# Optimization experiments

Measured on AMD Instinct MI355X. Metric: run time of the kernel, lower is better.

The kernel has to match this reference:

```python
import jax, jax.numpy as jnp
import numpy as np

ALPHA = 0.1
BETA = 0.25


def setup_inputs() -> dict:
    key = jax.random.key(0)
    k1, k2 = jax.random.split(key)
    B, C, D = 65536, 4096, 128
    x = jax.random.normal(k1, (B, D), dtype=jnp.float32)
    codes = jax.random.normal(k2, (1, C, D), dtype=jnp.float32)
    return {"x": x, "codes": codes}


def reference(x, codes):
    # x: [B, D], codes: [1, C, D]
    D = x.shape[1]
    c = codes[0]  # [C, D]
    d2 = (
        jnp.sum(x * x, axis=1, keepdims=True)
        + jnp.sum(c * c, axis=1)[None, :]
        - 2.0 * (x @ c.T)
    )  # [B, C]
    distances = jnp.sqrt(jnp.maximum(d2, 0.0)) / (D ** 0.5) / ALPHA
    indices = jnp.argmin(distances, axis=-1)  # [B]
    quantized = c[indices]  # [B, D] codebook gather
    loss_commit = jnp.mean(
        jnp.sum((x - jax.lax.stop_gradient(quantized)) ** 2, axis=-1)
    )
    loss_codebook = jnp.mean(
        jnp.sum((quantized - jax.lax.stop_gradient(x)) ** 2, axis=-1)
    )
    loss = loss_commit + BETA * loss_codebook
    return quantized, indices, loss
```

## Files before the change

kernel.cpp:

```cpp
#include <hip/hip_runtime.h>

constexpr int Bn = 65536;
constexpr int Cn = 4096;
constexpr int Dn = 128;
constexpr float TAU = 0.055f;

typedef _Float16 v8h __attribute__((ext_vector_type(8)));
typedef float v16f __attribute__((ext_vector_type(16)));

#define MFMA16(a, b, c) __builtin_amdgcn_mfma_f32_32x32x16_f16((a), (b), (c), 0, 0, 0)

__global__ void pack_codes_kernel(const float* __restrict__ codes,
                                  float* __restrict__ cnorm,
                                  _Float16* __restrict__ pack,
                                  float* __restrict__ codesT,
                                  int* __restrict__ flagcount) {
  int tid = blockIdx.x * 256 + threadIdx.x;
  if (tid == 0) *flagcount = 0;
  int f = tid >> 6;
  int l = tid & 63;
  int ct = f / 9, s = f % 9;
  int code = (ct << 5) + (l & 31);
  if (s < 8) {
    int kb = (s << 4) + ((l >> 5) << 3);
    const float* p = codes + (size_t)code * Dn + kb;
    float4 a = ((const float4*)p)[0];
    float4 b = ((const float4*)p)[1];
    float v[8] = {a.x, a.y, a.z, a.w, b.x, b.y, b.z, b.w};
#pragma unroll
    for (int j = 0; j < 8; ++j)
      codesT[(size_t)(kb + j) * Cn + code] = v[j];
    v8h hi;
#pragma unroll
    for (int j = 0; j < 8; ++j) {
      float sv = -2.f * v[j];
      hi[j] = (_Float16)sv;
    }
    *(v8h*)(pack + (size_t)ct * 4608 + s * 512 + l * 8) = hi;
  } else {
    v8h a = {0, 0, 0, 0, 0, 0, 0, 0};
    if (l < 32) {
      const float4* p = (const float4*)(codes + (size_t)code * Dn);
      double sd = 0.0;
#pragma unroll
      for (int i = 0; i < Dn / 4; ++i) {
        float4 v = p[i];
        sd += (double)v.x * v.x + (double)v.y * v.y + (double)v.z * v.z +
              (double)v.w * v.w;
      }
      float cn = (float)sd;
      cnorm[code] = cn;
      float c5 = cn + 512.f;
      _Float16 h1 = (_Float16)c5;
      float r1 = c5 - (float)h1;
      _Float16 h2 = (_Float16)r1;
      float r2 = r1 - (float)h2;
      _Float16 h3 = (_Float16)r2;
      a[0] = h1;
      a[1] = h2;
      a[2] = h3;
    }
    *(v8h*)(pack + (size_t)ct * 4608 + 8 * 512 + l * 8) = a;
  }
}

__launch_bounds__(256, 4)
__global__ void argmin_mfma_kernel(const float* __restrict__ x,
                                   const _Float16* __restrict__ pack,
                                   float* __restrict__ pm1,
                                   float* __restrict__ pm2,
                                   float* __restrict__ pidx) {
  __shared__ __align__(16) _Float16 packLDS[4][4608];

  const int t = threadIdx.x;
  const int w = t >> 6;
  const int l = t & 63;
  const int h = blockIdx.x & 3;
  const int row0 = (blockIdx.x >> 2) * 256;

  v8h xh[2][8];
#pragma unroll
  for (int tt = 0; tt < 2; ++tt) {
#pragma unroll
    for (int ks = 0; ks < 8; ++ks) {
      int xrow = row0 + w * 64 + tt * 32 + (l & 31);
      int kb = ks * 16 + (l >> 5) * 8;
      const float* xp = x + (size_t)xrow * Dn + kb;
      float4 a = ((const float4*)xp)[0];
      float4 b = ((const float4*)xp)[1];
      float v[8] = {a.x, a.y, a.z, a.w, b.x, b.y, b.z, b.w};
      v8h hh;
#pragma unroll
      for (int j = 0; j < 8; ++j) hh[j] = (_Float16)v[j];
      xh[tt][ks] = hh;
    }
  }

  v8h bones;
#pragma unroll
  for (int j = 0; j < 8; ++j)
    bones[j] = (l < 32 && j < 3) ? (_Float16)1.0f : (_Float16)0.0f;

  v16f zacc;
#pragma unroll
  for (int i = 0; i < 16; ++i) zacc[i] = 0.f;

  const char* packbase = (const char*)pack + (size_t)(h * 32) * 9216;
  auto stage = [&](int pt, int bank) {
    const char* src = packbase + (size_t)pt * 18432 + l * 16;
    char* dstb = (char*)&packLDS[bank * 2][0];
    for (int i = w; i < 18; i += 4) {
      __builtin_amdgcn_global_load_lds(
          (const __attribute__((address_space(1))) unsigned*)(src + i * 1024),
          (__attribute__((address_space(3))) unsigned*)(dstb + i * 1024), 16,
          0, 0);
    }
  };

  stage(0, 0);
  __syncthreads();

  unsigned umin1[2] = {0xFFFFFFFFu, 0xFFFFFFFFu};
  unsigned umin2[2] = {0xFFFFFFFFu, 0xFFFFFFFFu};
  int idx[2] = {0, 0};

  auto update = [&](const v16f& a, int tt, int codebase) {
    unsigned b[16];
#pragma unroll
    for (int r = 0; r < 16; ++r)
      b[r] = (__float_as_uint(a[r]) & 0xFFFFFFF0u) | (unsigned)r;
    unsigned m1 = 0xFFFFFFFFu, m2 = 0xFFFFFFFFu;
#pragma unroll
    for (int i = 0; i < 8; ++i) {
      unsigned lo = min(b[2 * i], b[2 * i + 1]);
      unsigned hi = max(b[2 * i], b[2 * i + 1]);
      unsigned mx = max(m1, lo);
      m1 = min(m1, lo);
      m2 = min(min(m2, hi), mx);
    }
    unsigned r1 = m1 & 15u;
    int tidx = codebase + (int)(8 * (r1 >> 2) + (r1 & 3));
    bool lt = m1 < umin1[tt];
    umin2[tt] = lt ? min(umin1[tt], m2) : min(umin2[tt], m1);
    idx[tt] = lt ? tidx : idx[tt];
    umin1[tt] = lt ? m1 : umin1[tt];
  };

  for (int it = 0; it < 16; ++it) {
    const int bank = it & 1;
    if (it + 1 < 16) stage(it + 1, bank ^ 1);

#pragma unroll
    for (int j = 0; j < 2; ++j) {
      const _Float16* base = &packLDS[bank * 2 + j][l * 8];
      v8h a_cn = *(const v8h*)(base + 8 * 512);
      v16f ini = MFMA16(a_cn, bones, zacc);
      v8h a_h0 = *(const v8h*)(base + 0 * 512);
      v16f acc0 = MFMA16(a_h0, xh[0][0], ini);
      v16f acc1 = MFMA16(a_h0, xh[1][0], ini);
#pragma unroll
      for (int s = 1; s < 8; ++s) {
        v8h a_h = *(const v8h*)(base + s * 512);
        acc0 = MFMA16(a_h, xh[0][s], acc0);
        acc1 = MFMA16(a_h, xh[1][s], acc1);
      }
      const int codebase = h * 1024 + (2 * it + j) * 32 + 4 * (l >> 5);
      update(acc0, 0, codebase);
      update(acc1, 1, codebase);
    }
    __syncthreads();
  }

#pragma unroll
  for (int tt = 0; tt < 2; ++tt) {
    unsigned o1 = (unsigned)__shfl_xor((int)umin1[tt], 32);
    unsigned o2 = (unsigned)__shfl_xor((int)umin2[tt], 32);
    int oi = __shfl_xor(idx[tt], 32);
    bool sw = (o1 < umin1[tt]) || (o1 == umin1[tt] && oi < idx[tt]);
    unsigned n1 = sw ? o1 : umin1[tt];
    int ni = sw ? oi : idx[tt];
    unsigned big = sw ? umin1[tt] : o1;
    unsigned n2 = min(min(umin2[tt], o2), big);
    if (l < 32) {
      int row = row0 + w * 64 + tt * 32 + l;
      pm1[h * Bn + row] = __uint_as_float(n1 & 0xFFFFFFF0u);
      pm2[h * Bn + row] = __uint_as_float(n2 & 0xFFFFFFF0u);
      pidx[h * Bn + row] = (float)ni;
    }
  }
}

__global__ void merge_kernel(const float* __restrict__ pm1,
                             const float* __restrict__ pm2,
                             const float* __restrict__ pidx,
                             float* __restrict__ idxf,
                             int* __restrict__ flaglist,
                             int* __restrict__ flagcount) {
  int r = blockIdx.x * 256 + threadIdx.x;
  float m1 = pm1[r];
  float mw2 = pm2[r];
  float mi = pidx[r];
  float m2 = 3.4e38f;
#pragma unroll
  for (int h = 1; h < 4; ++h) {
    float v1 = pm1[h * Bn + r];
    float v2 = pm2[h * Bn + r];
    float vi = pidx[h * Bn + r];
    bool win = v1 < m1;
    m2 = fminf(m2, win ? m1 : v1);
    mw2 = win ? v2 : mw2;
    mi = win ? vi : mi;
    m1 = win ? v1 : m1;
  }
  m2 = fminf(m2, mw2);
  idxf[r] = mi;
  if (m2 - m1 < TAU) {
    int p = atomicAdd(flagcount, 1);
    flaglist[p] = r;
  }
}

__global__ void rescore_part_kernel(const float* __restrict__ x,
                                    const float* __restrict__ codesT,
                                    const float* __restrict__ cnorm,
                                    const int* __restrict__ flaglist,
                                    const int* __restrict__ flagcount,
                                    float* __restrict__ prv,
                                    int* __restrict__ pri) {
  __shared__ __align__(16) float xrow[Dn];
  __shared__ float wv[4];
  __shared__ int wis[4];
  const int t = threadIdx.x;
  const int total = 4 * (*flagcount);

  for (int wi = blockIdx.x; wi < total; wi += gridDim.x) {
    const int j = wi >> 2;
    const int q = wi & 3;
    const int r = flaglist[j];
    __syncthreads();
    if (t < 32) ((float4*)xrow)[t] = ((const float4*)(x + (size_t)r * Dn))[t];
    __syncthreads();

    const int c0 = q * 1024 + 4 * t;
    const float* cp = codesT + c0;
    float4 s = {0.f, 0.f, 0.f, 0.f};
#pragma unroll 4
    for (int d = 0; d < Dn; ++d) {
      float xv = xrow[d];
      float4 cv = *(const float4*)(cp + (size_t)d * Cn);
      s.x = fmaf(cv.x, xv, s.x);
      s.y = fmaf(cv.y, xv, s.y);
      s.z = fmaf(cv.z, xv, s.z);
      s.w = fmaf(cv.w, xv, s.w);
    }
    float k0 = fmaf(-2.f, s.x, cnorm[c0]);
    float k1 = fmaf(-2.f, s.y, cnorm[c0 + 1]);
    float k2 = fmaf(-2.f, s.z, cnorm[c0 + 2]);
    float k3 = fmaf(-2.f, s.w, cnorm[c0 + 3]);
    float bv = k0;
    int bi = c0;
    if (k1 < bv) { bv = k1; bi = c0 + 1; }
    if (k2 < bv) { bv = k2; bi = c0 + 2; }
    if (k3 < bv) { bv = k3; bi = c0 + 3; }
#pragma unroll
    for (int off = 32; off > 0; off >>= 1) {
      float ov = __shfl_down(bv, off);
      int oi = __shfl_down(bi, off);
      if (ov < bv || (ov == bv && oi < bi)) { bv = ov; bi = oi; }
    }
    if ((t & 63) == 0) { wv[t >> 6] = bv; wis[t >> 6] = bi; }
    __syncthreads();
    if (t == 0) {
#pragma unroll
      for (int k = 1; k < 4; ++k) {
        if (wv[k] < bv || (wv[k] == bv && wis[k] < bi)) {
          bv = wv[k];
          bi = wis[k];
        }
      }
      prv[wi] = bv;
      pri[wi] = bi;
    }
  }
}

__global__ void rescore_final_kernel(const int* __restrict__ flaglist,
                                     const int* __restrict__ flagcount,
                                     const float* __restrict__ prv,
                                     const int* __restrict__ pri,
                                     float* __restrict__ idxf) {
  const int cnt = *flagcount;
  for (int j = blockIdx.x * blockDim.x + threadIdx.x; j < cnt;
       j += gridDim.x * blockDim.x) {
    float bv = prv[4 * j];
    int bi = pri[4 * j];
#pragma unroll
    for (int k = 1; k < 4; ++k) {
      float ov = prv[4 * j + k];
      int oi = pri[4 * j + k];
      if (ov < bv || (ov == bv && oi < bi)) { bv = ov; bi = oi; }
    }
    idxf[flaglist[j]] = (float)bi;
  }
}

__global__ void gather_loss_kernel(const float* __restrict__ x,
                                   const float* __restrict__ codes,
                                   const float* __restrict__ idxf,
                                   float* __restrict__ quant,
                                   float* __restrict__ partial) {
  __shared__ float part[8];
  const int t = threadIdx.x;
  const int wave = t >> 6;
  const int lane = t & 63;
  const int half = lane >> 5;
  const int l = lane & 31;
  const int base = blockIdx.x * 32;

  float s = 0.f;
#pragma unroll
  for (int pass = 0; pass < 4; ++pass) {
    int row = base + pass * 8 + (wave << 1) + half;
    int idx = (int)idxf[row];
    float4 cv = ((const float4*)(codes + (size_t)idx * Dn))[l];
    float4 xv = ((const float4*)(x + (size_t)row * Dn))[l];
    ((float4*)(quant + (size_t)row * Dn))[l] = cv;
    float d0 = xv.x - cv.x, d1 = xv.y - cv.y, d2 = xv.z - cv.z,
          d3 = xv.w - cv.w;
    s += d0 * d0 + d1 * d1 + d2 * d2 + d3 * d3;
  }
#pragma unroll
  for (int off = 16; off > 0; off >>= 1) s += __shfl_down(s, off, 32);
  if (l == 0) part[(wave << 1) + half] = s;
  __syncthreads();
  if (t == 0) {
    float tot = 0.f;
#pragma unroll
    for (int i = 0; i < 8; ++i) tot += part[i];
    partial[blockIdx.x] = tot;
  }
}

__global__ void loss_sum_kernel(const float* __restrict__ partial,
                                float* __restrict__ loss) {
  __shared__ float red[4];
  const int t = threadIdx.x;
  float s = 0.f;
  for (int i = t; i < 2048; i += 256) s += partial[i];
#pragma unroll
  for (int off = 32; off > 0; off >>= 1) s += __shfl_down(s, off, 64);
  if ((t & 63) == 0) red[t >> 6] = s;
  __syncthreads();
  if (t == 0)
    *loss = (red[0] + red[1] + red[2] + red[3]) * (1.25f / 65536.f);
}

extern "C" void kernel_launch(void* const* d_in, const int* in_sizes, int n_in,
                              void* d_out, int out_size, void* d_ws,
                              size_t ws_size, hipStream_t stream) {
  const float* x = (const float*)d_in[0];
  const float* codes = (const float*)d_in[1];

  float* quant = (float*)d_out;
  float* idxf = quant + (size_t)Bn * Dn;
  float* loss = idxf + Bn;
  float* cnorm = (float*)d_ws;
  float* partial = cnorm + Cn;

  _Float16* pack = (_Float16*)quant;
  int* flagcount = (int*)(quant + (1 << 20));
  int* flaglist = flagcount + 1;
  float* pm1 = quant + (2 << 20);
  float* pm2 = pm1 + 4 * Bn;
  float* pidx = pm2 + 4 * Bn;
  float* codesT = quant + (3 << 20);
  float* prv = quant + (4 << 20);
  int* pri = (int*)(quant + (4 << 20) + (1 << 18));

  pack_codes_kernel<<<288, 256, 0, stream>>>(codes, cnorm, pack, codesT,
                                             flagcount);
  argmin_mfma_kernel<<<1024, 256, 0, stream>>>(x, pack, pm1, pm2, pidx);
  merge_kernel<<<Bn / 256, 256, 0, stream>>>(pm1, pm2, pidx, idxf, flaglist,
                                             flagcount);
  rescore_part_kernel<<<2048, 256, 0, stream>>>(x, codesT, cnorm, flaglist,
                                                flagcount, prv, pri);
  rescore_final_kernel<<<64, 256, 0, stream>>>(flaglist, flagcount, prv, pri,
                                               idxf);
  gather_loss_kernel<<<Bn / 32, 256, 0, stream>>>(x, codes, idxf, quant,
                                                  partial);
  loss_sum_kernel<<<1, 256, 0, stream>>>(partial, loss);
}
```

Baseline: 235.4 us.

## Batch eight flagged rows per block in fp32 rescore to reuse codebook loads

The fp32 rescore kernel now processes eight flagged rows per work item, keeping eight accumulator sets so that each codesT load from global memory is reused across eight rows instead of one. This cuts codebook traffic for the rescore pass, which was bandwidth-bound re-reading the 2MB transposed codebook per flagged row. The partial-result layout and the final merge are updated to match, the grid is halved, and launch bounds are added. The cost is more registers per thread, and padded duplicate rows in the last batch.

Result: faster. 218.0 us (-7.4%).

```diff
diff --git a/kernel.cpp b/kernel.cpp
--- a/kernel.cpp
+++ b/kernel.cpp
@@ -220,6 +220,7 @@
   }
 }
 
+__launch_bounds__(256, 4)
 __global__ void rescore_part_kernel(const float* __restrict__ x,
                                     const float* __restrict__ codesT,
                                     const float* __restrict__ cnorm,
@@ -227,59 +228,92 @@
                                     const int* __restrict__ flagcount,
                                     float* __restrict__ prv,
                                     int* __restrict__ pri) {
-  __shared__ __align__(16) float xrow[Dn];
-  __shared__ float wv[4];
-  __shared__ int wis[4];
+  __shared__ __align__(16) float xs[8][Dn];
+  __shared__ float wv[4][8];
+  __shared__ int wis[4][8];
   const int t = threadIdx.x;
-  const int total = 4 * (*flagcount);
+  const int cnt = *flagcount;
+  const int nb = (cnt + 7) >> 3;
+  const int total = nb * 4;
 
   for (int wi = blockIdx.x; wi < total; wi += gridDim.x) {
-    const int j = wi >> 2;
+    const int b = wi >> 2;
     const int q = wi & 3;
-    const int r = flaglist[j];
     __syncthreads();
-    if (t < 32) ((float4*)xrow)[t] = ((const float4*)(x + (size_t)r * Dn))[t];
+    {
+      int rr = t >> 5;
+      int cc = t & 31;
+      int j = min(b * 8 + rr, cnt - 1);
+      int r = flaglist[j];
+      ((float4*)&xs[rr][0])[cc] = ((const float4*)(x + (size_t)r * Dn))[cc];
+    }
     __syncthreads();
 
     const int c0 = q * 1024 + 4 * t;
     const float* cp = codesT + c0;
-    float4 s = {0.f, 0.f, 0.f, 0.f};
-#pragma unroll 4
+    float4 s[8];
+#pragma unroll
+    for (int r = 0; r < 8; ++r) s[r] = (float4){0.f, 0.f, 0.f, 0.f};
     for (int d = 0; d < Dn; ++d) {
-      float xv = xrow[d];
       float4 cv = *(const float4*)(cp + (size_t)d * Cn);
-      s.x = fmaf(cv.x, xv, s.x);
-      s.y = fmaf(cv.y, xv, s.y);
-      s.z = fmaf(cv.z, xv, s.z);
-      s.w = fmaf(cv.w, xv, s.w);
-    }
-    float k0 = fmaf(-2.f, s.x, cnorm[c0]);
-    float k1 = fmaf(-2.f, s.y, cnorm[c0 + 1]);
-    float k2 = fmaf(-2.f, s.z, cnorm[c0 + 2]);
-    float k3 = fmaf(-2.f, s.w, cnorm[c0 + 3]);
-    float bv = k0;
-    int bi = c0;
-    if (k1 < bv) { bv = k1; bi = c0 + 1; }
-    if (k2 < bv) { bv = k2; bi = c0 + 2; }
-    if (k3 < bv) { bv = k3; bi = c0 + 3; }
-#pragma unroll
-    for (int off = 32; off > 0; off >>= 1) {
-      float ov = __shfl_down(bv, off);
-      int oi = __shfl_down(bi, off);
-      if (ov < bv || (ov == bv && oi < bi)) { bv = ov; bi = oi; }
-    }
-    if ((t & 63) == 0) { wv[t >> 6] = bv; wis[t >> 6] = bi; }
+#pragma unroll
+      for (int r = 0; r < 8; ++r) {
+        float xv = xs[r][d];
+        s[r].x = fmaf(cv.x, xv, s[r].x);
+        s[r].y = fmaf(cv.y, xv, s[r].y);
+        s[r].z = fmaf(cv.z, xv, s[r].z);
+        s[r].w = fmaf(cv.w, xv, s[r].w);
+      }
+    }
+    const float cn0 = cnorm[c0], cn1 = cnorm[c0 + 1], cn2 = cnorm[c0 + 2],
+                cn3 = cnorm[c0 + 3];
+    float bv[8];
+    int bi[8];
+#pragma unroll
+    for (int r = 0; r < 8; ++r) {
+      float k0 = fmaf(-2.f, s[r].x, cn0);
+      float k1 = fmaf(-2.f, s[r].y, cn1);
+      float k2 = fmaf(-2.f, s[r].z, cn2);
+      float k3 = fmaf(-2.f, s[r].w, cn3);
+      float v = k0;
+      int i = c0;
+      if (k1 < v) { v = k1; i = c0 + 1; }
+      if (k2 < v) { v = k2; i = c0 + 2; }
+      if (k3 < v) { v = k3; i = c0 + 3; }
+      bv[r] = v;
+      bi[r] = i;
+    }
+#pragma unroll
+    for (int r = 0; r < 8; ++r) {
+#pragma unroll
+      for (int off = 32; off > 0; off >>= 1) {
+        float ov = __shfl_down(bv[r], off);
+        int oi = __shfl_down(bi[r], off);
+        if (ov < bv[r] || (ov == bv[r] && oi < bi[r])) {
+          bv[r] = ov;
+          bi[r] = oi;
+        }
+      }
+    }
+    if ((t & 63) == 0) {
+#pragma unroll
+      for (int r = 0; r < 8; ++r) {
+        wv[t >> 6][r] = bv[r];
+        wis[t >> 6][r] = bi[r];
+      }
+    }
     __syncthreads();
-    if (t == 0) {
+    if (t < 8) {
+      float v = wv[0][t];
+      int i = wis[0][t];
 #pragma unroll
       for (int k = 1; k < 4; ++k) {
-        if (wv[k] < bv || (wv[k] == bv && wis[k] < bi)) {
-          bv = wv[k];
-          bi = wis[k];
-        }
-      }
-      prv[wi] = bv;
-      pri[wi] = bi;
+        float ov = wv[k][t];
+        int oi = wis[k][t];
+        if (ov < v || (ov == v && oi < i)) { v = ov; i = oi; }
+      }
+      prv[wi * 8 + t] = v;
+      pri[wi * 8 + t] = i;
     }
   }
 }
@@ -292,12 +326,14 @@
   const int cnt = *flagcount;
   for (int j = blockIdx.x * blockDim.x + threadIdx.x; j < cnt;
        j += gridDim.x * blockDim.x) {
-    float bv = prv[4 * j];
-    int bi = pri[4 * j];
+    const int b = j >> 3;
+    const int rr = j & 7;
+    float bv = prv[(b * 4 + 0) * 8 + rr];
+    int bi = pri[(b * 4 + 0) * 8 + rr];
 #pragma unroll
     for (int k = 1; k < 4; ++k) {
-      float ov = prv[4 * j + k];
-      int oi = pri[4 * j + k];
+      float ov = prv[(b * 4 + k) * 8 + rr];
+      int oi = pri[(b * 4 + k) * 8 + rr];
       if (ov < bv || (ov == bv && oi < bi)) { bv = ov; bi = oi; }
     }
     idxf[flaglist[j]] = (float)bi;
@@ -382,7 +418,7 @@
   argmin_mfma_kernel<<<1024, 256, 0, stream>>>(x, pack, pm1, pm2, pidx);
   merge_kernel<<<Bn / 256, 256, 0, stream>>>(pm1, pm2, pidx, idxf, flaglist,
                                              flagcount);
-  rescore_part_kernel<<<2048, 256, 0, stream>>>(x, codesT, cnorm, flaglist,
+  rescore_part_kernel<<<1024, 256, 0, stream>>>(x, codesT, cnorm, flaglist,
                                                 flagcount, prv, pri);
   rescore_final_kernel<<<64, 256, 0, stream>>>(flaglist, flagcount, prv, pri,
                                                idxf);
```
